# Kernel tuning notes

Measured on AMD Instinct MI355X. Metric: run time of the kernel, lower is better.

## Reference

```python
import jax, jax.numpy as jnp
import numpy as np

N_NODES = 10000
N_EDGES = 160000
DIM = 128
NLAYERS = 3
NBASIS = 16
NSPECIES = 100
CUTOFF = 5.0


def _mlp(x, W1, b1, W2, b2):
    # FullyConnectedNet([hidden, out]) with silu on hidden, linear output
    return jax.nn.silu(x @ W1 + b1) @ W2 + b2


def setup_inputs() -> dict:
    key = jax.random.key(0)
    ks = iter(jax.random.split(key, 64))
    scale = 0.08

    def w(shape):
        return jax.random.normal(next(ks), shape, dtype=jnp.float32) * scale

    inp = {
        "species": jax.random.randint(next(ks), (N_NODES,), 0, NSPECIES, dtype=jnp.int32),
        "edge_src": jnp.sort(jax.random.randint(next(ks), (N_EDGES,), 0, N_NODES, dtype=jnp.int32)),
        "edge_dst": jax.random.randint(next(ks), (N_EDGES,), 0, N_NODES, dtype=jnp.int32),
        "distances": 0.5 + 4.4 * jax.random.uniform(next(ks), (N_EDGES,), dtype=jnp.float32),
        "vec": jax.random.normal(next(ks), (N_EDGES, 3), dtype=jnp.float32),
        "switch": jax.random.uniform(next(ks), (N_EDGES,), dtype=jnp.float32),
        "species_W": w((NSPECIES, DIM)),
        "species_b": w((DIM,)),
        "radial_W": w((NLAYERS, NBASIS, DIM)),
        "radial_b": w((NLAYERS, DIM)),
    }
    for nm, out in [("a", DIM), ("F", 1), ("f", DIM), ("R", DIM), ("r", DIM), ("u", DIM)]:
        inp[nm + "_W1"] = w((NLAYERS, DIM, DIM))
        inp[nm + "_b1"] = w((NLAYERS, DIM))
        inp[nm + "_W2"] = w((NLAYERS, DIM, out))
        inp[nm + "_b2"] = w((NLAYERS, out))
    return inp


def reference(species, edge_src, edge_dst, distances, vec, switch,
              species_W, species_b, radial_W, radial_b,
              a_W1, a_b1, a_W2, a_b2,
              F_W1, F_b1, F_W2, F_b2,
              f_W1, f_b1, f_W2, f_b2,
              R_W1, R_b1, R_W2, R_b2,
              r_W1, r_b1, r_W2, r_b2,
              u_W1, u_b1, u_W2, u_b2):
    N = species.shape[0]
    # species encoding -> species_linear Dense
    xi = jax.nn.one_hot(species, NSPECIES, dtype=jnp.float32) @ species_W + species_b  # (N, dim)
    sw = switch[:, None]                                   # (E, 1)
    dirij = vec / distances[:, None] * sw                  # (E, 3)
    # gaussian radial basis on [0, cutoff]
    centers = jnp.linspace(0.0, CUTOFF, NBASIS, dtype=jnp.float32)
    eta = jnp.float32((NBASIS / CUTOFF) ** 2)
    rb = jnp.exp(-eta * (distances[:, None] - centers) ** 2)  # (E, nbasis)

    fi = None
    di = None
    for l in range(NLAYERS):
        ai = _mlp(xi, a_W1[l], a_b1[l], a_W2[l], a_b2[l])          # (N, dim)
        Dij = rb @ radial_W[l] + radial_b[l]                        # (E, dim)
        mij = ai[edge_src] * ai[edge_dst] * Dij * sw                # (E, dim)
        xi = xi + jax.ops.segment_sum(mij, edge_src, N)
        Fij = _mlp(mij, F_W1[l], F_b1[l], F_W2[l], F_b2[l]) * dirij  # (E, 3)
        fij = _mlp(mij, f_W1[l], f_b1[l], f_W2[l], f_b2[l])[:, :, None] * Fij[:, None, :]  # (E, C, 3)
        fij_sum = jax.ops.segment_sum(fij, edge_src, N)             # (N, C, 3)
        fi = fij_sum if l == 0 else fi + fij_sum
        deltai = _mlp(xi, R_W1[l], R_b1[l], R_W2[l], R_b2[l])[:, :, None] * fi  # (N, C, 3)
        if l == 0:
            di = deltai
        else:
            phi_rij = _mlp(mij, r_W1[l], r_b1[l], r_W2[l], r_b2[l])  # (E, C)
            phi_r = jax.ops.segment_sum(phi_rij * sw, edge_src, N)   # (N, C)
            di = phi_r[:, :, None] * di + deltai
        scal = jnp.sum(fi * di, axis=-1)                             # (N, C)
        dui = -_mlp(xi, u_W1[l], u_b1[l], u_W2[l], u_b2[l]) * scal   # (N, dim) since C == dim
        xi = xi + dui
    return xi
```

## Files before the change

kernel.cpp:

```cpp
#include <hip/hip_runtime.h>
#include <hip/hip_bf16.h>

#define N_NODES 10000
#define N_EDGES 160000
#define DIM     128
#define NBASIS  16
#define LDT     136
#define NFE     (N_NODES*DIM)

typedef __bf16 bf16x8 __attribute__((ext_vector_type(8)));
typedef __bf16 bf16x4 __attribute__((ext_vector_type(4)));
typedef __bf16 bf16x2 __attribute__((ext_vector_type(2)));
typedef float  f32x4  __attribute__((ext_vector_type(4)));

__device__ __forceinline__ float silu_f(float x){
  return x * (1.0f / (1.0f + __expf(-x)));
}
__device__ __forceinline__ f32x4 mfma16(bf16x8 a, bf16x8 b, f32x4 c){
  return __builtin_amdgcn_mfma_f32_16x16x32_bf16(a,b,c,0,0,0);
}


struct WPtrs { const float* p[11]; };

template<bool WITH_R>
__global__ __launch_bounds__(256,2) void mlp_layer(
    int nodeB,
    const __bf16* __restrict__ mij,
    const int*    __restrict__ esrc, const float* __restrict__ dirv,
    const __bf16* __restrict__ fW1z, const float* __restrict__ fb1,
    const __bf16* __restrict__ fW2z, const float* __restrict__ fb2,
    const __bf16* __restrict__ FW1z, const float* __restrict__ Fb1,
    const float*  __restrict__ FW2v, const float* __restrict__ Fb2,
    const __bf16* __restrict__ rW1z, const float* __restrict__ rb1,
    const __bf16* __restrict__ rW2z, const float* __restrict__ rb2,
    const float*  __restrict__ swv,
    float* __restrict__ fiG, float* __restrict__ phiG,
    const float* __restrict__ X,
    const __bf16* __restrict__ RW1z, const float* __restrict__ Rb1,
    const __bf16* __restrict__ RW2z, const float* __restrict__ Rb2,
    const __bf16* __restrict__ uW1z, const float* __restrict__ ub1,
    const __bf16* __restrict__ uW2z, const float* __restrict__ ub2,
    float* __restrict__ Rv, float* __restrict__ uv)
{
  __shared__ __bf16 sH[128*LDT];
  __shared__ __bf16 sW[2][8192];
  __shared__ int    sE[128];
  __shared__ float  sDir[128*3];
  const int tid=threadIdx.x, lane=tid&63, wv=tid>>6, l15=lane&15, quad=lane>>4;

  if ((int)blockIdx.x < nodeB){
    const long row0n = (long)blockIdx.x*64 + wv*16;
    const long rA = row0n + l15;
    const bool okA = rA < N_NODES;

    bf16x8 fa[4];
    #pragma unroll
    for (int kc=0;kc<4;kc++){
      int kb=kc*32+quad*8;
      bf16x8 a;
      #pragma unroll
      for (int i=0;i<8;i++) a[i]=(__bf16)0.f;
      if (okA){
        float4 u0 = *(const float4*)(X + rA*DIM + kb);
        float4 u1 = *(const float4*)(X + rA*DIM + kb + 4);
        a[0]=(__bf16)u0.x;a[1]=(__bf16)u0.y;a[2]=(__bf16)u0.z;a[3]=(__bf16)u0.w;
        a[4]=(__bf16)u1.x;a[5]=(__bf16)u1.y;a[6]=(__bf16)u1.z;a[7]=(__bf16)u1.w;
      }
      fa[kc]=a;
    }

    f32x4 acc[8];
    auto zacc = [&](){
      #pragma unroll
      for (int ni=0;ni<8;++ni) acc[ni]=(f32x4){0.f,0.f,0.f,0.f};
    };
    auto gemmA = [&](const __bf16* __restrict__ Wz){
      #pragma unroll
      for (int kc=0;kc<4;kc++){
        #pragma unroll
        for (int ni=0;ni<8;ni++){
          bf16x8 w = *(const bf16x8*)(Wz + (long)(kc*512 + ni*64 + lane)*8);
          acc[ni]=mfma16(w,fa[kc],acc[ni]);
        }
      }
    };
    auto gemmH = [&](const __bf16* __restrict__ Wz){
      #pragma unroll
      for (int kc=0;kc<4;kc++){
        bf16x8 h0=*(bf16x8*)&sH[(wv*16+l15)*LDT + kc*32 + quad*8];
        #pragma unroll
        for (int ni=0;ni<8;ni++){
          bf16x8 w = *(const bf16x8*)(Wz + (long)(kc*512 + ni*64 + lane)*8);
          acc[ni]=mfma16(w,h0,acc[ni]);
        }
      }
    };
    auto hEpi = [&](const float* __restrict__ b1){
      #pragma unroll
      for (int ni=0;ni<8;++ni){
        int n0 = ni*16 + quad*4;
        float4 bb = *(const float4*)(b1 + n0);
        bf16x4 h;
        h[0]=(__bf16)silu_f(acc[ni][0]+bb.x);
        h[1]=(__bf16)silu_f(acc[ni][1]+bb.y);
        h[2]=(__bf16)silu_f(acc[ni][2]+bb.z);
        h[3]=(__bf16)silu_f(acc[ni][3]+bb.w);
        *(bf16x4*)&sH[(wv*16+l15)*LDT + n0] = h;
      }
    };
    auto cStoreF = [&](const float* __restrict__ b2, float* __restrict__ Y){
      if (okA){
        #pragma unroll
        for (int ni=0;ni<8;++ni){
          int n0 = ni*16 + quad*4;
          float4 bb = *(const float4*)(b2 + n0);
          float4 o;
          o.x=acc[ni][0]+bb.x; o.y=acc[ni][1]+bb.y;
          o.z=acc[ni][2]+bb.z; o.w=acc[ni][3]+bb.w;
          *(float4*)(Y + rA*DIM + n0) = o;
        }
      }
    };

    zacc(); gemmA(RW1z); hEpi(Rb1);
    zacc(); gemmH(RW2z); cStoreF(Rb2, Rv);
    zacc(); gemmA(uW1z); hEpi(ub1);
    zacc(); gemmH(uW2z); cStoreF(ub2, uv);
    return;
  }

  const long row0 = (long)(blockIdx.x - nodeB)*128;
  const int  rloc0 = wv*32 + l15;
  const long rB0 = row0 + rloc0, rB1 = rB0+16;

  if (tid < 32)  *(int4*)&sE[tid*4]    = *(const int4*)(esrc + row0 + tid*4);
  if (tid >= 64 && tid < 160)
    *(float4*)&sDir[(tid-64)*4] = *(const float4*)(dirv + row0*3 + (tid-64)*4);

  bf16x8 fb[2][4];
  #pragma unroll
  for (int kc=0;kc<4;kc++){
    fb[0][kc] = *(const bf16x8*)(mij + rB0*DIM + kc*32 + quad*8);
    fb[1][kc] = *(const bf16x8*)(mij + rB1*DIM + kc*32 + quad*8);
  }
  float swr[2];
  if constexpr (WITH_R){ swr[0]=swv[rB0]; swr[1]=swv[rB1]; }

  f32x4 acc[2][8];
  bf16x8 pre[4];
  float eF[2];

  auto preload = [&](const __bf16* __restrict__ Wz, int half){
    #pragma unroll
    for (int it=0; it<4; ++it)
      pre[it] = *(const bf16x8*)(Wz + (long)(half*1024 + it*256 + tid)*8);
  };
  auto writePre = [&](int b){
    #pragma unroll
    for (int it=0; it<4; ++it)
      *(bf16x8*)&sW[b][(it*256+tid)*8] = pre[it];
  };
  auto zacc = [&](){
    #pragma unroll
    for (int mi=0;mi<2;++mi)
      #pragma unroll
      for (int ni=0;ni<8;++ni) acc[mi][ni]=(f32x4){0.f,0.f,0.f,0.f};
  };
  auto mfmaB = [&](int b, int half){
    #pragma unroll
    for (int k2=0;k2<2;k2++){
      int kc = half*2 + k2;
      #pragma unroll
      for (int ni=0;ni<8;ni++){
        bf16x8 w = *(bf16x8*)&sW[b][(k2*512 + ni*64 + lane)*8];
        acc[0][ni]=mfma16(w,fb[0][kc],acc[0][ni]);
        acc[1][ni]=mfma16(w,fb[1][kc],acc[1][ni]);
      }
    }
  };
  auto mfmaH = [&](int b, int half){
    #pragma unroll
    for (int k2=0;k2<2;k2++){
      int kc = half*2 + k2;
      bf16x8 h0=*(bf16x8*)&sH[(rloc0   )*LDT + kc*32 + quad*8];
      bf16x8 h1=*(bf16x8*)&sH[(rloc0+16)*LDT + kc*32 + quad*8];
      #pragma unroll
      for (int ni=0;ni<8;ni++){
        bf16x8 w = *(bf16x8*)&sW[b][(k2*512 + ni*64 + lane)*8];
        acc[0][ni]=mfma16(w,h0,acc[0][ni]);
        acc[1][ni]=mfma16(w,h1,acc[1][ni]);
      }
    }
  };
  auto fEpi = [&](){
    float fb2v = Fb2[0];
    #pragma unroll
    for (int mi=0;mi<2;++mi){
      float p = 0.f;
      #pragma unroll
      for (int ni=0;ni<8;++ni){
        int n0 = ni*16 + quad*4;
        float4 bb = *(const float4*)(Fb1 + n0);
        float4 w2 = *(const float4*)(FW2v + n0);
        p += silu_f(acc[mi][ni][0]+bb.x)*w2.x;
        p += silu_f(acc[mi][ni][1]+bb.y)*w2.y;
        p += silu_f(acc[mi][ni][2]+bb.z)*w2.z;
        p += silu_f(acc[mi][ni][3]+bb.w)*w2.w;
      }
      p += __shfl_xor(p,16);
      p += __shfl_xor(p,32);
      eF[mi] = p + fb2v;
    }
  };
  auto hEpi = [&](const float* __restrict__ b1){
    #pragma unroll
    for (int mi=0;mi<2;++mi){
      int rl = wv*32 + mi*16 + l15;
      #pragma unroll
      for (int ni=0;ni<8;++ni){
        int n0 = ni*16 + quad*4;
        float4 bb = *(const float4*)(b1 + n0);
        bf16x4 h;
        h[0]=(__bf16)silu_f(acc[mi][ni][0]+bb.x);
        h[1]=(__bf16)silu_f(acc[mi][ni][1]+bb.y);
        h[2]=(__bf16)silu_f(acc[mi][ni][2]+bb.z);
        h[3]=(__bf16)silu_f(acc[mi][ni][3]+bb.w);
        *(bf16x4*)&sH[rl*LDT + n0] = h;
      }
    }
  };
  auto outLDS = [&](const float* __restrict__ b2, const float* mul){
    #pragma unroll
    for (int mi=0;mi<2;++mi){
      int rl = wv*32 + mi*16 + l15;
      #pragma unroll
      for (int ni=0;ni<8;++ni){
        int n0 = ni*16 + quad*4;
        float4 bb = *(const float4*)(b2 + n0);
        bf16x4 o;
        o[0]=(__bf16)((acc[mi][ni][0]+bb.x)*mul[mi]);
        o[1]=(__bf16)((acc[mi][ni][1]+bb.y)*mul[mi]);
        o[2]=(__bf16)((acc[mi][ni][2]+bb.z)*mul[mi]);
        o[3]=(__bf16)((acc[mi][ni][3]+bb.w)*mul[mi]);
        *(bf16x4*)&sH[rl*LDT + n0] = o;
      }
    }
  };
  auto reduceFi = [&](){
    const int d = lane*2;
    float a0=0.f,a1=0.f,a2=0.f,a3=0.f,a4=0.f,a5=0.f;
    int cur = sE[wv*32];
    for (int i=0;i<32;i++){
      int e = wv*32+i;
      int n = sE[e];
      if (n != cur){
        long b = (long)cur*DIM + d;
        atomicAdd(&fiG[0L*NFE + b  ], a0);
        atomicAdd(&fiG[0L*NFE + b+1], a3);
        atomicAdd(&fiG[1L*NFE + b  ], a1);
        atomicAdd(&fiG[1L*NFE + b+1], a4);
        atomicAdd(&fiG[2L*NFE + b  ], a2);
        atomicAdd(&fiG[2L*NFE + b+1], a5);
        a0=a1=a2=a3=a4=a5=0.f; cur=n;
      }
      bf16x2 v = *(bf16x2*)&sH[e*LDT + d];
      float vx=(float)v[0], vy=(float)v[1];
      float d0=sDir[e*3+0], d1=sDir[e*3+1], d2=sDir[e*3+2];
      a0+=vx*d0; a1+=vx*d1; a2+=vx*d2;
      a3+=vy*d0; a4+=vy*d1; a5+=vy*d2;
    }
    long b = (long)cur*DIM + d;
    atomicAdd(&fiG[0L*NFE + b  ], a0);
    atomicAdd(&fiG[0L*NFE + b+1], a3);
    atomicAdd(&fiG[1L*NFE + b  ], a1);
    atomicAdd(&fiG[1L*NFE + b+1], a4);
    atomicAdd(&fiG[2L*NFE + b  ], a2);
    atomicAdd(&fiG[2L*NFE + b+1], a5);
  };
  auto reducePhi = [&](){
    const int d = lane*2;
    float a0=0.f,a1=0.f;
    int cur = sE[wv*32];
    for (int i=0;i<32;i++){
      int e = wv*32+i;
      int n = sE[e];
      if (n != cur){
        atomicAdd(&phiG[(long)cur*DIM + d  ], a0);
        atomicAdd(&phiG[(long)cur*DIM + d+1], a1);
        a0=a1=0.f; cur=n;
      }
      bf16x2 v = *(bf16x2*)&sH[e*LDT + d];
      a0 += (float)v[0]; a1 += (float)v[1];
    }
    atomicAdd(&phiG[(long)cur*DIM + d  ], a0);
    atomicAdd(&phiG[(long)cur*DIM + d+1], a1);
  };

  preload(FW1z,0); writePre(0);
  __syncthreads();
  preload(FW1z,1);
  zacc(); mfmaB(0,0);
  writePre(1);
  __syncthreads();
  preload(fW1z,0);
  mfmaB(1,1);
  writePre(0);
  __syncthreads();
  preload(fW1z,1);
  fEpi();
  zacc(); mfmaB(0,0);
  writePre(1);
  __syncthreads();
  preload(fW2z,0);
  mfmaB(1,1);
  writePre(0);
  __syncthreads();
  preload(fW2z,1);
  hEpi(fb1);
  zacc(); mfmaH(0,0);
  writePre(1);
  __syncthreads();
  if constexpr (WITH_R) preload(rW1z,0);
  mfmaH(1,1);
  outLDS(fb2, eF);
  reduceFi();

  if constexpr (WITH_R){
    writePre(0);
    __syncthreads();
    preload(rW1z,1);
    zacc(); mfmaB(0,0);
    writePre(1);
    __syncthreads();
    preload(rW2z,0);
    mfmaB(1,1);
    writePre(0);
    __syncthreads();
    preload(rW2z,1);
    hEpi(rb1);
    zacc(); mfmaH(0,0);
    writePre(1);
    __syncthreads();
    mfmaH(1,1);
    outLDS(rb2, swr);
    reducePhi();
  }
}

__global__ __launch_bounds__(64,4) void mlp_a(
    const float* __restrict__ X,
    const __bf16* __restrict__ W1z, const float* __restrict__ b1,
    const __bf16* __restrict__ W2z, const float* __restrict__ b2,
    __bf16* __restrict__ Y)
{
  __shared__ __bf16 sH[16*LDT];
  const int lane=threadIdx.x, l15=lane&15, quad=lane>>4;
  const long row0=(long)blockIdx.x*16;
  const long rA=row0+l15;

  bf16x8 fa[4];
  #pragma unroll
  for (int kc=0;kc<4;kc++){
    int kb=kc*32+quad*8;
    float4 u0 = *(const float4*)(X + rA*DIM + kb);
    float4 u1 = *(const float4*)(X + rA*DIM + kb + 4);
    bf16x8 a;
    a[0]=(__bf16)u0.x;a[1]=(__bf16)u0.y;a[2]=(__bf16)u0.z;a[3]=(__bf16)u0.w;
    a[4]=(__bf16)u1.x;a[5]=(__bf16)u1.y;a[6]=(__bf16)u1.z;a[7]=(__bf16)u1.w;
    fa[kc]=a;
  }

  f32x4 acc[8];
  #pragma unroll
  for (int ni=0;ni<8;++ni) acc[ni]=(f32x4){0.f,0.f,0.f,0.f};
  #pragma unroll
  for (int kc=0;kc<4;kc++){
    #pragma unroll
    for (int ni=0;ni<8;ni++){
      bf16x8 w = *(const bf16x8*)(W1z + (long)(kc*512 + ni*64 + lane)*8);
      acc[ni]=mfma16(w,fa[kc],acc[ni]);
    }
  }
  #pragma unroll
  for (int ni=0;ni<8;++ni){
    int n0 = ni*16 + quad*4;
    float4 bb = *(const float4*)(b1 + n0);
    bf16x4 h;
    h[0]=(__bf16)silu_f(acc[ni][0]+bb.x);
    h[1]=(__bf16)silu_f(acc[ni][1]+bb.y);
    h[2]=(__bf16)silu_f(acc[ni][2]+bb.z);
    h[3]=(__bf16)silu_f(acc[ni][3]+bb.w);
    *(bf16x4*)&sH[l15*LDT + n0] = h;
  }
  #pragma unroll
  for (int ni=0;ni<8;++ni) acc[ni]=(f32x4){0.f,0.f,0.f,0.f};
  #pragma unroll
  for (int kc=0;kc<4;kc++){
    bf16x8 h0=*(bf16x8*)&sH[l15*LDT + kc*32 + quad*8];
    #pragma unroll
    for (int ni=0;ni<8;ni++){
      bf16x8 w = *(const bf16x8*)(W2z + (long)(kc*512 + ni*64 + lane)*8);
      acc[ni]=mfma16(w,h0,acc[ni]);
    }
  }
  #pragma unroll
  for (int ni=0;ni<8;++ni){
    int n0 = ni*16 + quad*4;
    float4 bb = *(const float4*)(b2 + n0);
    bf16x4 o;
    o[0]=(__bf16)(acc[ni][0]+bb.x);
    o[1]=(__bf16)(acc[ni][1]+bb.y);
    o[2]=(__bf16)(acc[ni][2]+bb.z);
    o[3]=(__bf16)(acc[ni][3]+bb.w);
    *(bf16x4*)(Y + rA*DIM + n0) = o;
  }
}

__global__ __launch_bounds__(256) void setup_all(
    WPtrs wp, __bf16* __restrict__ wt,
    const int* __restrict__ species, const float* __restrict__ spW,
    const float* __restrict__ spB, float* __restrict__ xi, float* __restrict__ fi,
    float* __restrict__ phi,
    const float* __restrict__ dist, const float* __restrict__ vec,
    const float* __restrict__ swv, float* __restrict__ dir, float* __restrict__ rb)
{
  const int b = blockIdx.x, tid = threadIdx.x;
  if (b < 33){
    int t = b/3, l = b%3;
    const float* src = wp.p[t] + (size_t)l*16384;
    __bf16* out = wt + (size_t)b*16384;
    for (int it=0; it<8; ++it){
      int fi_ = it*256 + tid;
      int kc = fi_>>9, ni = (fi_>>6)&7, lane = fi_&63;
      int n  = ni*16 + (lane&15);
      int k0 = kc*32 + (lane>>4)*8;
      bf16x8 v;
      #pragma unroll
      for (int j=0;j<8;++j) v[j] = (__bf16)src[(k0+j)*DIM + n];
      *(bf16x8*)(out + (size_t)fi_*8) = v;
    }
  } else if (b < 33 + 5000){
    int idx = (b-33)*256 + tid;
    int n = idx >> 7, d = idx & 127;
    xi[idx] = spW[species[n]*DIM + d] + spB[d];
    phi[idx] = 0.f;
    fi[idx] = 0.f;
    fi[NFE + idx] = 0.f;
    fi[2L*NFE + idx] = 0.f;
  } else {
    int e = (b-5033)*256 + tid;
    if (e < N_EDGES){
      float d = dist[e];
      float s = swv[e];
      float inv = s / d;
      dir[e*3+0] = vec[e*3+0]*inv;
      dir[e*3+1] = vec[e*3+1]*inv;
      dir[e*3+2] = vec[e*3+2]*inv;
      const float eta = (16.0f/5.0f)*(16.0f/5.0f);
      #pragma unroll
      for (int j=0;j<NBASIS;j++){
        float c = (float)j * (5.0f/15.0f);
        float t2 = d - c;
        rb[e*NBASIS + j] = __expf(-eta*t2*t2);
      }
    }
  }
}

__global__ __launch_bounds__(256) void mij_segsum(
    const __bf16* __restrict__ ai, const int* __restrict__ esrc, const int* __restrict__ edst,
    const float* __restrict__ swv, const float* __restrict__ rb,
    const float* __restrict__ radW, const float* __restrict__ radB,
    __bf16* __restrict__ mij, float* __restrict__ xi)
{
  __shared__ float sRb[64*NBASIS];
  __shared__ int   sS[64], sD[64];
  __shared__ float sSw[64];
  int tid = threadIdx.x;
  int e0 = blockIdx.x * 64;
  *(float4*)(sRb + tid*4) = *(const float4*)(rb + (long)e0*NBASIS + tid*4);
  if (tid < 64){
    sS[tid]  = esrc[e0+tid];
    sD[tid]  = edst[e0+tid];
    sSw[tid] = swv[e0+tid];
  }
  const int wv = tid>>6, lane = tid&63;
  const int d = lane*2;
  float2 rw[NBASIS];
  #pragma unroll
  for (int j=0;j<NBASIS;j++)
    rw[j] = *(const float2*)(radW + j*DIM + d);
  float2 rB = *(const float2*)(radB + d);
  __syncthreads();

  float sx=0.f, sy=0.f;
  int cur = sS[wv*16];
  #pragma unroll
  for (int i=0;i<16;i++){
    int el = wv*16 + i;
    int n = sS[el];
    if (n != cur){
      atomicAdd(&xi[(long)cur*DIM+d  ], sx);
      atomicAdd(&xi[(long)cur*DIM+d+1], sy);
      sx=0.f; sy=0.f; cur=n;
    }
    bf16x2 as = *(const bf16x2*)(ai + (long)n*DIM + d);
    bf16x2 ad = *(const bf16x2*)(ai + (long)sD[el]*DIM + d);
    float acc0 = 0.f, acc1 = 0.f;
    #pragma unroll
    for (int j=0;j<NBASIS;j++){
      float rbv = sRb[el*NBASIS+j];
      acc0 += rbv*rw[j].x;
      acc1 += rbv*rw[j].y;
    }
    float sw_ = sSw[el];
    float m0 = (float)as[0]*(float)ad[0]*(acc0+rB.x)*sw_;
    float m1 = (float)as[1]*(float)ad[1]*(acc1+rB.y)*sw_;
    bf16x2 m; m[0]=(__bf16)m0; m[1]=(__bf16)m1;
    *(bf16x2*)(mij + (long)(e0+el)*DIM + d) = m;
    sx += m0; sy += m1;
  }
  atomicAdd(&xi[(long)cur*DIM+d  ], sx);
  atomicAdd(&xi[(long)cur*DIM+d+1], sy);
}

__global__ __launch_bounds__(256) void node_update(
    const float* __restrict__ Rv, const float* __restrict__ uv,
    float* __restrict__ fi, float* __restrict__ di, float* __restrict__ xi,
    float* __restrict__ phi, float* __restrict__ out, int layer)
{
  long idx = (long)blockIdx.x*256 + threadIdx.x;
  float f0 = fi[idx];
  float f1 = fi[NFE + idx];
  float f2 = fi[2L*NFE + idx];
  float phi_v = (layer > 0) ? phi[idx] : 0.f;
  float Rv_ = Rv[idx];
  float fv[3] = {f0,f1,f2};
  float sc = 0.f;
  #pragma unroll
  for (int k=0;k<3;k++){
    float delta = Rv_*fv[k];
    float dv = (layer==0) ? delta : phi_v*di[(long)k*NFE + idx] + delta;
    di[(long)k*NFE + idx] = dv;
    sc += fv[k]*dv;
  }
  float nx = xi[idx] - uv[idx]*sc;
  xi[idx] = nx;
  phi[idx] = 0.f;
  if (layer == 2) out[idx] = nx;
}

extern "C" void kernel_launch(void* const* d_in, const int* in_sizes, int n_in,
                              void* d_out, int out_size, void* d_ws, size_t ws_size,
                              hipStream_t stream) {
  const int*   species = (const int*)  d_in[0];
  const int*   esrc    = (const int*)  d_in[1];
  const int*   edst    = (const int*)  d_in[2];
  const float* dist    = (const float*)d_in[3];
  const float* vec     = (const float*)d_in[4];
  const float* swv     = (const float*)d_in[5];
  const float* spW     = (const float*)d_in[6];
  const float* spB     = (const float*)d_in[7];
  const float* radW    = (const float*)d_in[8];
  const float* radB    = (const float*)d_in[9];
  const float* aW1=(const float*)d_in[10], *aB1=(const float*)d_in[11], *aW2=(const float*)d_in[12], *aB2=(const float*)d_in[13];
  const float* FW1=(const float*)d_in[14], *FB1=(const float*)d_in[15], *FW2=(const float*)d_in[16], *FB2=(const float*)d_in[17];
  const float* fW1=(const float*)d_in[18], *fB1=(const float*)d_in[19], *fW2=(const float*)d_in[20], *fB2=(const float*)d_in[21];
  const float* RW1=(const float*)d_in[22], *RB1=(const float*)d_in[23], *RW2=(const float*)d_in[24], *RB2=(const float*)d_in[25];
  const float* rW1=(const float*)d_in[26], *rB1=(const float*)d_in[27], *rW2=(const float*)d_in[28], *rB2=(const float*)d_in[29];
  const float* uW1=(const float*)d_in[30], *uB1=(const float*)d_in[31], *uW2=(const float*)d_in[32], *uB2=(const float*)d_in[33];

  const long NF = (long)N_NODES*DIM;
  const long EF = (long)N_EDGES*DIM;
  float* ws   = (float*)d_ws;
  float* xi   = ws;
  float* Rv   = xi   + NF;
  float* uv   = Rv   + NF;
  float* phi  = uv   + NF;
  float* fi   = phi  + NF;
  float* di   = fi   + 3*NF;
  float* dir  = di   + 3*NF;
  float* rb   = dir  + 3L*N_EDGES;
  char* bp = (char*)(rb + 16L*N_EDGES);
  size_t off = ((size_t)(bp - (char*)d_ws) + 15) & ~(size_t)15;
  __bf16* ai   = (__bf16*)((char*)d_ws + off);
  __bf16* mij  = ai  + NF;
  __bf16* wt   = mij + EF;

  WPtrs wp;
  wp.p[0]=aW1; wp.p[1]=aW2; wp.p[2]=FW1; wp.p[3]=fW1; wp.p[4]=fW2;
  wp.p[5]=RW1; wp.p[6]=RW2; wp.p[7]=rW1; wp.p[8]=rW2; wp.p[9]=uW1; wp.p[10]=uW2;

  setup_all<<<5658, 256, 0, stream>>>(wp, wt,
                                      species, spW, spB, xi, fi, phi,
                                      dist, vec, swv, dir, rb);

  const int nodeB = (N_NODES + 63)/64;
  const int edgeB = N_EDGES/128;
  #define WT(t,l) (wt + (size_t)((t)*3+(l))*16384)

  for (int l=0;l<3;l++){
    const long bo = (long)l*DIM;

    mlp_a<<<N_NODES/16, 64, 0, stream>>>(xi, WT(0,l), aB1+bo, WT(1,l), aB2+bo, ai);
    mij_segsum<<<N_EDGES/64, 256, 0, stream>>>(ai, esrc, edst, swv, rb,
                                               radW + (long)l*NBASIS*DIM, radB + bo,
                                               mij, xi);
    if (l == 0)
      mlp_layer<false><<<nodeB+edgeB, 256, 0, stream>>>(
          nodeB, mij, esrc, dir,
          WT(3,l), fB1+bo, WT(4,l), fB2+bo,
          WT(2,l), FB1+bo, FW2+(long)l*DIM, FB2+l,
          nullptr, nullptr, nullptr, nullptr, nullptr,
          fi, phi,
          xi, WT(5,l), RB1+bo, WT(6,l), RB2+bo,
          WT(9,l), uB1+bo, WT(10,l), uB2+bo, Rv, uv);
    else
      mlp_layer<true><<<nodeB+edgeB, 256, 0, stream>>>(
          nodeB, mij, esrc, dir,
          WT(3,l), fB1+bo, WT(4,l), fB2+bo,
          WT(2,l), FB1+bo, FW2+(long)l*DIM, FB2+l,
          WT(7,l), rB1+bo, WT(8,l), rB2+bo, swv,
          fi, phi,
          xi, WT(5,l), RB1+bo, WT(6,l), RB2+bo,
          WT(9,l), uB1+bo, WT(10,l), uB2+bo, Rv, uv);
    node_update<<<5000, 256, 0, stream>>>(Rv, uv, fi, di, xi, phi,
                                          (float*)d_out, l);
  }
}
```

Measured before the change: 505.3 us.

## Stream MLP weights in quarter-K chunks to shrink LDS and raise occupancy

Result: slower. 519.0 us (+2.7%).

```diff
diff --git a/kernel.cpp b/kernel.cpp
--- a/kernel.cpp
+++ b/kernel.cpp
@@ -24,7 +24,7 @@
 struct WPtrs { const float* p[11]; };
 
 template<bool WITH_R>
-__global__ __launch_bounds__(256,2) void mlp_layer(
+__global__ __launch_bounds__(256,3) void mlp_layer(
     int nodeB,
     const __bf16* __restrict__ mij,
     const int*    __restrict__ esrc, const float* __restrict__ dirv,
@@ -44,7 +44,7 @@
     float* __restrict__ Rv, float* __restrict__ uv)
 {
   __shared__ __bf16 sH[128*LDT];
-  __shared__ __bf16 sW[2][8192];
+  __shared__ __bf16 sW[2][4096];
   __shared__ int    sE[128];
   __shared__ float  sDir[128*3];
   const int tid=threadIdx.x, lane=tid&63, wv=tid>>6, l15=lane&15, quad=lane>>4;
@@ -148,17 +148,17 @@
   if constexpr (WITH_R){ swr[0]=swv[rB0]; swr[1]=swv[rB1]; }
 
   f32x4 acc[2][8];
-  bf16x8 pre[4];
+  bf16x8 pre[2];
   float eF[2];
 
-  auto preload = [&](const __bf16* __restrict__ Wz, int half){
-    #pragma unroll
-    for (int it=0; it<4; ++it)
-      pre[it] = *(const bf16x8*)(Wz + (long)(half*1024 + it*256 + tid)*8);
+  auto preload = [&](const __bf16* __restrict__ Wz, int q){
+    #pragma unroll
+    for (int it=0; it<2; ++it)
+      pre[it] = *(const bf16x8*)(Wz + (long)(q*512 + it*256 + tid)*8);
   };
   auto writePre = [&](int b){
     #pragma unroll
-    for (int it=0; it<4; ++it)
+    for (int it=0; it<2; ++it)
       *(bf16x8*)&sW[b][(it*256+tid)*8] = pre[it];
   };
   auto zacc = [&](){
@@ -167,30 +167,22 @@
       #pragma unroll
       for (int ni=0;ni<8;++ni) acc[mi][ni]=(f32x4){0.f,0.f,0.f,0.f};
   };
-  auto mfmaB = [&](int b, int half){
-    #pragma unroll
-    for (int k2=0;k2<2;k2++){
-      int kc = half*2 + k2;
-      #pragma unroll
-      for (int ni=0;ni<8;ni++){
-        bf16x8 w = *(bf16x8*)&sW[b][(k2*512 + ni*64 + lane)*8];
-        acc[0][ni]=mfma16(w,fb[0][kc],acc[0][ni]);
-        acc[1][ni]=mfma16(w,fb[1][kc],acc[1][ni]);
-      }
-    }
-  };
-  auto mfmaH = [&](int b, int half){
-    #pragma unroll
-    for (int k2=0;k2<2;k2++){
-      int kc = half*2 + k2;
-      bf16x8 h0=*(bf16x8*)&sH[(rloc0   )*LDT + kc*32 + quad*8];
-      bf16x8 h1=*(bf16x8*)&sH[(rloc0+16)*LDT + kc*32 + quad*8];
-      #pragma unroll
-      for (int ni=0;ni<8;ni++){
-        bf16x8 w = *(bf16x8*)&sW[b][(k2*512 + ni*64 + lane)*8];
-        acc[0][ni]=mfma16(w,h0,acc[0][ni]);
-        acc[1][ni]=mfma16(w,h1,acc[1][ni]);
-      }
+  auto mfmaB = [&](int b, int kc){
+    #pragma unroll
+    for (int ni=0;ni<8;ni++){
+      bf16x8 w = *(bf16x8*)&sW[b][(ni*64 + lane)*8];
+      acc[0][ni]=mfma16(w,fb[0][kc],acc[0][ni]);
+      acc[1][ni]=mfma16(w,fb[1][kc],acc[1][ni]);
+    }
+  };
+  auto mfmaH = [&](int b, int kc){
+    bf16x8 h0=*(bf16x8*)&sH[(rloc0   )*LDT + kc*32 + quad*8];
+    bf16x8 h1=*(bf16x8*)&sH[(rloc0+16)*LDT + kc*32 + quad*8];
+    #pragma unroll
+    for (int ni=0;ni<8;ni++){
+      bf16x8 w = *(bf16x8*)&sW[b][(ni*64 + lane)*8];
+      acc[0][ni]=mfma16(w,h0,acc[0][ni]);
+      acc[1][ni]=mfma16(w,h1,acc[1][ni]);
     }
   };
   auto fEpi = [&](){
@@ -297,55 +289,50 @@
     atomicAdd(&phiG[(long)cur*DIM + d+1], a1);
   };
 
+  int buf = 0;
   preload(FW1z,0); writePre(0);
   __syncthreads();
+
+  zacc();
   preload(FW1z,1);
-  zacc(); mfmaB(0,0);
-  writePre(1);
-  __syncthreads();
-  preload(fW1z,0);
-  mfmaB(1,1);
-  writePre(0);
-  __syncthreads();
-  preload(fW1z,1);
+  mfmaB(0,0);
+  writePre(1); __syncthreads(); preload(FW1z,2); mfmaB(1,1);
+  writePre(0); __syncthreads(); preload(FW1z,3); mfmaB(0,2);
+  writePre(1); __syncthreads(); preload(fW1z,0); mfmaB(1,3);
+  writePre(0); __syncthreads(); preload(fW1z,1);
   fEpi();
   zacc(); mfmaB(0,0);
-  writePre(1);
-  __syncthreads();
-  preload(fW2z,0);
-  mfmaB(1,1);
-  writePre(0);
-  __syncthreads();
-  preload(fW2z,1);
+  writePre(1); __syncthreads(); preload(fW1z,2); mfmaB(1,1);
+  writePre(0); __syncthreads(); preload(fW1z,3); mfmaB(0,2);
+  writePre(1); __syncthreads(); preload(fW2z,0); mfmaB(1,3);
+  writePre(0); __syncthreads(); preload(fW2z,1);
   hEpi(fb1);
   zacc(); mfmaH(0,0);
-  writePre(1);
-  __syncthreads();
+  writePre(1); __syncthreads(); preload(fW2z,2); mfmaH(1,1);
+  writePre(0); __syncthreads(); preload(fW2z,3); mfmaH(0,2);
+  writePre(1); __syncthreads();
   if constexpr (WITH_R) preload(rW1z,0);
-  mfmaH(1,1);
+  mfmaH(1,3);
   outLDS(fb2, eF);
   reduceFi();
 
   if constexpr (WITH_R){
-    writePre(0);
-    __syncthreads();
-    preload(rW1z,1);
+    writePre(0); __syncthreads(); preload(rW1z,1);
     zacc(); mfmaB(0,0);
-    writePre(1);
-    __syncthreads();
-    preload(rW2z,0);
-    mfmaB(1,1);
-    writePre(0);
-    __syncthreads();
-    preload(rW2z,1);
+    writePre(1); __syncthreads(); preload(rW1z,2); mfmaB(1,1);
+    writePre(0); __syncthreads(); preload(rW1z,3); mfmaB(0,2);
+    writePre(1); __syncthreads(); preload(rW2z,0); mfmaB(1,3);
+    writePre(0); __syncthreads(); preload(rW2z,1);
     hEpi(rb1);
     zacc(); mfmaH(0,0);
-    writePre(1);
-    __syncthreads();
-    mfmaH(1,1);
+    writePre(1); __syncthreads(); preload(rW2z,2); mfmaH(1,1);
+    writePre(0); __syncthreads(); preload(rW2z,3); mfmaH(0,2);
+    writePre(1); __syncthreads();
+    mfmaH(1,3);
     outLDS(rb2, swr);
     reducePhi();
   }
+  (void)buf;
 }
 
 __global__ __launch_bounds__(64,4) void mlp_a(
```
